# Performance work log

Measured on AMD Instinct MI355X. Metric: run time of the kernel, lower is better.

The kernel has to match this reference:

```python
import jax, jax.numpy as jnp
import numpy as np

B, L, D = 32, 128, 512

def setup_inputs() -> dict:
    key = jax.random.key(0)
    ks = jax.random.split(key, 10)
    s = 1.0 / np.sqrt(D)
    return {
        "current_sotw": jax.random.normal(ks[0], (B, L, D), jnp.float32),
        "new_obs": jax.random.normal(ks[1], (B, L, D), jnp.float32),
        "Wq": jax.random.uniform(ks[2], (D, D), jnp.float32, -s, s),   # linear_query weight
        "bq": jax.random.uniform(ks[3], (D,), jnp.float32, -s, s),     # linear_query bias
        "Wc": jax.random.uniform(ks[4], (D, D), jnp.float32, -s, s),   # linear_context (no bias)
        "v": jax.random.uniform(ks[5], (D,), jnp.float32, -s, s),      # v projection to scalar score
        "Wout": jax.random.uniform(ks[6], (2 * D, D), jnp.float32, -s, s),  # linear_out weight
        "bout": jax.random.uniform(ks[7], (D,), jnp.float32, -s, s),        # linear_out bias (mlp type)
        "mix": jax.random.uniform(ks[8], (1,), jnp.float32),           # mixing_proportion ~ U[0,1)
    }

def _global_attn_mlp(source, memory, Wq, bq, Wc, v, Wout, bout):
    # OpenNMT GlobalAttention, attn_type='mlp', attn_func='softmax'
    wq = jnp.einsum('btd,de->bte', source, Wq) + bq          # [B,T,D]
    uh = jnp.einsum('bsd,de->bse', memory, Wc)               # [B,S,D]
    # scores: v . tanh(wq + uh) over broadcast [B,T,S,D]
    scores = jnp.einsum('btsd,d->bts', jnp.tanh(wq[:, :, None, :] + uh[:, None, :, :]), v)
    align = jax.nn.softmax(scores, axis=-1)                  # [B,T,S]
    c = jnp.einsum('bts,bsd->btd', align, memory)            # context [B,T,D]
    attn_h = jnp.einsum('btd,de->bte', jnp.concatenate([c, source], axis=-1), Wout) + bout
    return attn_h  # [B,T,D] (the torch code transposes to [T,B,D] then back)

def reference(current_sotw, new_obs, Wq, bq, Wc, v, Wout, bout, mix):
    a1 = _global_attn_mlp(new_obs, current_sotw, Wq, bq, Wc, v, Wout, bout)
    a2 = _global_attn_mlp(current_sotw, new_obs, Wq, bq, Wc, v, Wout, bout)
    m = mix[0]
    return (1.0 - m) * a1 + m * a2
```

## Files before the change

### kernel.cpp

```cpp
#include <hip/hip_runtime.h>

#define DD 512
#define SS 128
#define TT4 4
#define SCH16 16
#define RW 520
#define C2F 2.8853900817779268f
#define L2EF 1.4426950408889634f

typedef __bf16 bf16x8 __attribute__((ext_vector_type(8)));
typedef float f32x4 __attribute__((ext_vector_type(4)));
typedef unsigned int uint32x4 __attribute__((ext_vector_type(4)));

__device__ __forceinline__ unsigned short f2bf(float f) {
    unsigned int u = __builtin_bit_cast(unsigned int, f);
    u += 0x7fffu + ((u >> 16) & 1u);
    return (unsigned short)(u >> 16);
}
__device__ __forceinline__ float bflo(unsigned int u) { return __builtin_bit_cast(float, u << 16); }
__device__ __forceinline__ float bfhi(unsigned int u) { return __builtin_bit_cast(float, u & 0xffff0000u); }

__global__ __launch_bounds__(256)
void cvt_dual(const float* __restrict__ a, const float* __restrict__ b,
              unsigned short* __restrict__ oa, unsigned short* __restrict__ ob, int n8)
{
    int i = blockIdx.x * 256 + threadIdx.x;
    const float* in; unsigned short* out; int k;
    if (i < n8) { in = a; out = oa; k = i; }
    else        { in = b; out = ob; k = i - n8; }
    const float4 x = ((const float4*)in)[2 * k];
    const float4 y = ((const float4*)in)[2 * k + 1];
    uint32x4 o;
    o[0] = (unsigned)f2bf(x.x) | ((unsigned)f2bf(x.y) << 16);
    o[1] = (unsigned)f2bf(x.z) | ((unsigned)f2bf(x.w) << 16);
    o[2] = (unsigned)f2bf(y.x) | ((unsigned)f2bf(y.y) << 16);
    o[3] = (unsigned)f2bf(y.z) | ((unsigned)f2bf(y.w) << 16);
    ((uint32x4*)out)[k] = o;
}

__global__ __launch_bounds__(256)
void transpose_all(const float* __restrict__ Wq, const float* __restrict__ Wc,
                   const float* __restrict__ Wout,
                   unsigned short* __restrict__ Wqct, unsigned short* __restrict__ Woutt)
{
    __shared__ float t[64][65];
    const int z = blockIdx.z;
    const float* in; unsigned short* out; int R, r0;
    if (z == 0)      { in = Wq;   out = Wqct;             R = 512;  r0 = blockIdx.y * 64; }
    else if (z == 1) { in = Wc;   out = Wqct + 512 * 512; R = 512;  r0 = blockIdx.y * 64; }
    else             { in = Wout; out = Woutt;            R = 1024; r0 = (z - 2) * 512 + blockIdx.y * 64; }
    const int c0 = blockIdx.x * 64;
    const int tid = threadIdx.x;
    const int lc = tid & 63, lr = tid >> 6;
    #pragma unroll
    for (int i = 0; i < 16; ++i) {
        int r = lr + i * 4;
        t[r][lc] = in[(size_t)(r0 + r) * 512 + c0 + lc];
    }
    __syncthreads();
    #pragma unroll
    for (int i = 0; i < 16; ++i) {
        int rr = lr + i * 4;
        out[(size_t)(c0 + rr) * R + r0 + lc] = f2bf(t[lc][rr]);
    }
}

__global__ __launch_bounds__(256)
void gemm_proj(const unsigned short* __restrict__ A0, const unsigned short* __restrict__ A1,
               const unsigned short* __restrict__ Bt, const float* __restrict__ bq,
               unsigned short* __restrict__ w0, unsigned short* __restrict__ u0,
               unsigned short* __restrict__ w1, unsigned short* __restrict__ u1)
{
    constexpr int K = 512, LDA = 72;
    __shared__ __align__(16) unsigned short As[128][LDA];
    __shared__ __align__(16) unsigned short Bs[128][LDA];

    const unsigned short* A = blockIdx.z ? A1 : A0;
    unsigned short* outW    = blockIdx.z ? w1 : w0;
    unsigned short* outU    = blockIdx.z ? u1 : u0;

    const int tid = threadIdx.x;
    const int n0 = blockIdx.x * 128, m0 = blockIdx.y * 128;
    const int lane = tid & 63, wid = tid >> 6;
    const int wr = wid >> 1, wc = wid & 1;
    const int lr = lane & 15, kb = lane >> 4;

    f32x4 acc[4][4] = {};
    uint32x4 ra[4], rb[4];

    auto LOADK = [&](int k0) {
        #pragma unroll
        for (int j = 0; j < 4; ++j) {
            int id = tid + 256 * j; int r = id >> 3, s = id & 7;
            ra[j] = *(const uint32x4*)&A[(size_t)(m0 + r) * K + k0 + s * 8];
            rb[j] = *(const uint32x4*)&Bt[(size_t)(n0 + r) * K + k0 + s * 8];
        }
    };

    LOADK(0);
    #pragma unroll 1
    for (int step = 0; step < K / 64; ++step) {
        __syncthreads();
        #pragma unroll
        for (int j = 0; j < 4; ++j) {
            int id = tid + 256 * j; int r = id >> 3, s = id & 7;
            *(uint32x4*)&As[r][s * 8] = ra[j];
            *(uint32x4*)&Bs[r][s * 8] = rb[j];
        }
        __syncthreads();
        if (step + 1 < K / 64) LOADK((step + 1) * 64);
        #pragma unroll
        for (int kk = 0; kk < 64; kk += 32) {
            bf16x8 bfr[4];
            #pragma unroll
            for (int nf = 0; nf < 4; ++nf)
                bfr[nf] = __builtin_bit_cast(bf16x8, *(const uint32x4*)&Bs[wc * 64 + nf * 16 + lr][kk + kb * 8]);
            #pragma unroll
            for (int mf = 0; mf < 4; ++mf) {
                bf16x8 a0 = __builtin_bit_cast(bf16x8, *(const uint32x4*)&As[wr * 64 + mf * 16 + lr][kk + kb * 8]);
                #pragma unroll
                for (int nf = 0; nf < 4; ++nf)
                    acc[mf][nf] = __builtin_amdgcn_mfma_f32_16x16x32_bf16(a0, bfr[nf], acc[mf][nf], 0, 0, 0);
            }
        }
    }

    #pragma unroll
    for (int nf = 0; nf < 4; ++nf) {
        const int col = n0 + wc * 64 + nf * 16 + lr;
        const float bv = (col < 512) ? bq[col] : 0.0f;
        #pragma unroll
        for (int mf = 0; mf < 4; ++mf) {
            const int row = m0 + wr * 64 + mf * 16 + kb * 4;
            #pragma unroll
            for (int r = 0; r < 4; ++r) {
                const float valf = acc[mf][nf][r];
                if (col < 512) outW[(size_t)(row + r) * 512 + col] = f2bf((valf + bv) * C2F);
                else           outU[(size_t)(row + r) * 512 + (col - 512)] = f2bf(valf * C2F);
            }
        }
    }
}

__global__ __launch_bounds__(256)
void gemm_final(const unsigned short* __restrict__ c1, const unsigned short* __restrict__ c2,
                const float* __restrict__ no, const float* __restrict__ cs,
                const float* __restrict__ mix, const unsigned short* __restrict__ Bt,
                const float* __restrict__ bout, float* __restrict__ out)
{
    constexpr int K = 1024, LDA = 72;
    __shared__ __align__(16) unsigned short As[128][LDA];
    __shared__ __align__(16) unsigned short Bs[64][LDA];

    const int tid = threadIdx.x;
    const int n0 = blockIdx.x * 64, m0 = blockIdx.y * 128;
    const int lane = tid & 63, wid = tid >> 6;
    const int wr = wid >> 1, wc = wid & 1;
    const int lr = lane & 15, kb = lane >> 4;
    const float mxv = mix[0], omv = 1.0f - mxv;

    f32x4 acc[4][2] = {};
    uint32x4 ra[4], rb[2];

    auto LOADK = [&](int k0) {
        #pragma unroll
        for (int j = 0; j < 4; ++j) {
            int id = tid + 256 * j; int r = id >> 3, s = id & 7;
            const size_t row = m0 + r;
            const int k = k0 + s * 8;
            uint32x4 o;
            if (k < 512) {
                const uint32x4 x1 = *(const uint32x4*)&c1[row * 512 + k];
                const uint32x4 x2 = *(const uint32x4*)&c2[row * 512 + k];
                #pragma unroll
                for (int q = 0; q < 4; ++q) {
                    float lo = omv * bflo(x1[q]) + mxv * bflo(x2[q]);
                    float hi = omv * bfhi(x1[q]) + mxv * bfhi(x2[q]);
                    o[q] = (unsigned)f2bf(lo) | ((unsigned)f2bf(hi) << 16);
                }
            } else {
                const float* n1 = &no[row * 512 + k - 512];
                const float* s1 = &cs[row * 512 + k - 512];
                const float4 a1 = *(const float4*)n1, a2 = *(const float4*)(n1 + 4);
                const float4 b1 = *(const float4*)s1, b2 = *(const float4*)(s1 + 4);
                o[0] = (unsigned)f2bf(omv * a1.x + mxv * b1.x) | ((unsigned)f2bf(omv * a1.y + mxv * b1.y) << 16);
                o[1] = (unsigned)f2bf(omv * a1.z + mxv * b1.z) | ((unsigned)f2bf(omv * a1.w + mxv * b1.w) << 16);
                o[2] = (unsigned)f2bf(omv * a2.x + mxv * b2.x) | ((unsigned)f2bf(omv * a2.y + mxv * b2.y) << 16);
                o[3] = (unsigned)f2bf(omv * a2.z + mxv * b2.z) | ((unsigned)f2bf(omv * a2.w + mxv * b2.w) << 16);
            }
            ra[j] = o;
        }
        #pragma unroll
        for (int j = 0; j < 2; ++j) {
            int id = tid + 256 * j; int r = id >> 3, s = id & 7;
            rb[j] = *(const uint32x4*)&Bt[(size_t)(n0 + r) * K + k0 + s * 8];
        }
    };

    LOADK(0);
    #pragma unroll 1
    for (int step = 0; step < K / 64; ++step) {
        __syncthreads();
        #pragma unroll
        for (int j = 0; j < 4; ++j) {
            int id = tid + 256 * j; int r = id >> 3, s = id & 7;
            *(uint32x4*)&As[r][s * 8] = ra[j];
        }
        #pragma unroll
        for (int j = 0; j < 2; ++j) {
            int id = tid + 256 * j; int r = id >> 3, s = id & 7;
            *(uint32x4*)&Bs[r][s * 8] = rb[j];
        }
        __syncthreads();
        if (step + 1 < K / 64) LOADK((step + 1) * 64);
        #pragma unroll
        for (int kk = 0; kk < 64; kk += 32) {
            bf16x8 b0 = __builtin_bit_cast(bf16x8, *(const uint32x4*)&Bs[wc * 32 + lr][kk + kb * 8]);
            bf16x8 b1 = __builtin_bit_cast(bf16x8, *(const uint32x4*)&Bs[wc * 32 + 16 + lr][kk + kb * 8]);
            #pragma unroll
            for (int mf = 0; mf < 4; ++mf) {
                bf16x8 a0 = __builtin_bit_cast(bf16x8, *(const uint32x4*)&As[wr * 64 + mf * 16 + lr][kk + kb * 8]);
                acc[mf][0] = __builtin_amdgcn_mfma_f32_16x16x32_bf16(a0, b0, acc[mf][0], 0, 0, 0);
                acc[mf][1] = __builtin_amdgcn_mfma_f32_16x16x32_bf16(a0, b1, acc[mf][1], 0, 0, 0);
            }
        }
    }

    #pragma unroll
    for (int nf = 0; nf < 2; ++nf) {
        const int col = n0 + wc * 32 + nf * 16 + lr;
        const float bv = bout[col];
        #pragma unroll
        for (int mf = 0; mf < 4; ++mf) {
            const int row = m0 + wr * 64 + mf * 16 + kb * 4;
            #pragma unroll
            for (int r = 0; r < 4; ++r)
                out[(size_t)(row + r) * 512 + col] = acc[mf][nf][r] + bv;
        }
    }
}

__global__ __launch_bounds__(512, 8)
void attn_fused(const unsigned short* __restrict__ wq,
                const unsigned short* __restrict__ uh,
                const float* __restrict__ v,
                const unsigned short* __restrict__ mem,
                unsigned short* __restrict__ c_out)
{
    __shared__ __align__(16) unsigned short s_ew[TT4 * RW];
    __shared__ __align__(16) unsigned short s_eu[SCH16 * RW];
    __shared__ __align__(16) unsigned short s_v2[DD];
    __shared__ __align__(16) float s_sc[TT4 * SS];

    const int b = blockIdx.y, t0 = blockIdx.x * TT4;
    const int tid = threadIdx.x;

    if (tid < 256) {
        const int row = tid >> 6, G = tid & 63;
        const uint32x4 w4 = *(const uint32x4*)&wq[((size_t)b * SS + t0 + row) * DD + G * 8];
        uint32x4 o;
        #pragma unroll
        for (int q = 0; q < 4; ++q) {
            const float e0 = __builtin_amdgcn_exp2f(bflo(w4[q]));
            const float e1 = __builtin_amdgcn_exp2f(bfhi(w4[q]));
            o[q] = (unsigned)f2bf(e0) | ((unsigned)f2bf(e1) << 16);
        }
        *(uint32x4*)&s_ew[row * RW + G * 8] = o;
    } else if (tid < 320) {
        const int H = tid - 256;
        const float4 p = *(const float4*)&v[H * 8];
        const float4 q = *(const float4*)&v[H * 8 + 4];
        uint32x4 o;
        o[0] = (unsigned)f2bf(p.x * 2.f) | ((unsigned)f2bf(p.y * 2.f) << 16);
        o[1] = (unsigned)f2bf(p.z * 2.f) | ((unsigned)f2bf(p.w * 2.f) << 16);
        o[2] = (unsigned)f2bf(q.x * 2.f) | ((unsigned)f2bf(q.y * 2.f) << 16);
        o[3] = (unsigned)f2bf(q.z * 2.f) | ((unsigned)f2bf(q.w * 2.f) << 16);
        *(uint32x4*)&s_v2[H * 8] = o;
    }

    const int oct = tid & 7;
    const int sr  = (tid >> 3) & 15;
    const int t   = tid >> 7;

    for (int sc0 = 0; sc0 < SS; sc0 += SCH16) {
        __syncthreads();
        {
            int i = tid;
            #pragma unroll
            for (int rep = 0; rep < 2; ++rep, i += 512) {
                const int row = i >> 6, G = i & 63;
                const uint32x4 u4 = *(const uint32x4*)&uh[((size_t)b * SS + sc0 + row) * DD + G * 8];
                uint32x4 o;
                #pragma unroll
                for (int q = 0; q < 4; ++q) {
                    const unsigned e0 = __builtin_bit_cast(unsigned, __builtin_amdgcn_exp2f(bflo(u4[q])));
                    const unsigned e1 = __builtin_bit_cast(unsigned, __builtin_amdgcn_exp2f(bfhi(u4[q])));
                    o[q] = (e0 >> 16) | (e1 & 0xffff0000u);
                }
                *(uint32x4*)&s_eu[row * RW + G * 8] = o;
            }
        }
        __syncthreads();

        const unsigned short* wrow = &s_ew[t * RW];
        const unsigned short* urow = &s_eu[sr * RW];

        float a0 = 0.f, a1 = 0.f, a2 = 0.f, a3 = 0.f;
        #pragma unroll
        for (int j = 0; j < 8; ++j) {
            const int ch = (8 * j + oct) * 8;
            const uint32x4 w4 = *(const uint32x4*)&wrow[ch];
            const uint32x4 u4 = *(const uint32x4*)&urow[ch];
            const uint32x4 v4 = *(const uint32x4*)&s_v2[ch];
            a0 = fmaf(bflo(v4[0]), __builtin_amdgcn_rcpf(fmaf(bflo(w4[0]), bflo(u4[0]), 1.f)), a0);
            a1 = fmaf(bfhi(v4[0]), __builtin_amdgcn_rcpf(fmaf(bfhi(w4[0]), bfhi(u4[0]), 1.f)), a1);
            a2 = fmaf(bflo(v4[1]), __builtin_amdgcn_rcpf(fmaf(bflo(w4[1]), bflo(u4[1]), 1.f)), a2);
            a3 = fmaf(bfhi(v4[1]), __builtin_amdgcn_rcpf(fmaf(bfhi(w4[1]), bfhi(u4[1]), 1.f)), a3);
            a0 = fmaf(bflo(v4[2]), __builtin_amdgcn_rcpf(fmaf(bflo(w4[2]), bflo(u4[2]), 1.f)), a0);
            a1 = fmaf(bfhi(v4[2]), __builtin_amdgcn_rcpf(fmaf(bfhi(w4[2]), bfhi(u4[2]), 1.f)), a1);
            a2 = fmaf(bflo(v4[3]), __builtin_amdgcn_rcpf(fmaf(bflo(w4[3]), bflo(u4[3]), 1.f)), a2);
            a3 = fmaf(bfhi(v4[3]), __builtin_amdgcn_rcpf(fmaf(bfhi(w4[3]), bfhi(u4[3]), 1.f)), a3);
        }
        float p = (a0 + a1) + (a2 + a3);
        p += __shfl_xor(p, 1);
        p += __shfl_xor(p, 2);
        p += __shfl_xor(p, 4);
        if (oct == 0) s_sc[t * SS + sc0 + sr] = -p;
    }
    __syncthreads();

    if (tid < 128) {
        const int tr = tid >> 5, l32 = tid & 31;
        float x0 = s_sc[tr * SS + l32];
        float x1 = s_sc[tr * SS + l32 + 32];
        float x2 = s_sc[tr * SS + l32 + 64];
        float x3 = s_sc[tr * SS + l32 + 96];
        float mx = fmaxf(fmaxf(x0, x1), fmaxf(x2, x3));
        #pragma unroll
        for (int off = 16; off > 0; off >>= 1) mx = fmaxf(mx, __shfl_xor(mx, off));
        const float e0 = __builtin_amdgcn_exp2f((x0 - mx) * L2EF);
        const float e1 = __builtin_amdgcn_exp2f((x1 - mx) * L2EF);
        const float e2 = __builtin_amdgcn_exp2f((x2 - mx) * L2EF);
        const float e3 = __builtin_amdgcn_exp2f((x3 - mx) * L2EF);
        float sum = (e0 + e1) + (e2 + e3);
        #pragma unroll
        for (int off = 16; off > 0; off >>= 1) sum += __shfl_xor(sum, off);
        const float rs = __builtin_amdgcn_rcpf(sum);
        s_sc[tr * SS + l32]      = e0 * rs;
        s_sc[tr * SS + l32 + 32] = e1 * rs;
        s_sc[tr * SS + l32 + 64] = e2 * rs;
        s_sc[tr * SS + l32 + 96] = e3 * rs;
    }
    __syncthreads();

    {
        const int w = tid >> 6, lane = tid & 63;
        const int tb = w & 3, half = w >> 2;
        const int d = half * 256 + lane * 4;
        const unsigned short* mb = mem + (size_t)b * SS * DD + d;
        f32x4 ac = {0.f, 0.f, 0.f, 0.f};
        #pragma unroll 1
        for (int s = 0; s < SS; s += 4) {
            const float4 e4 = *(const float4*)&s_sc[tb * SS + s];
            #pragma unroll
            for (int q = 0; q < 4; ++q) {
                const float e = (q == 0) ? e4.x : (q == 1) ? e4.y : (q == 2) ? e4.z : e4.w;
                const uint2 mv = *(const uint2*)&mb[(size_t)(s + q) * DD];
                ac[0] = fmaf(e, bflo(mv.x), ac[0]);
                ac[1] = fmaf(e, bfhi(mv.x), ac[1]);
                ac[2] = fmaf(e, bflo(mv.y), ac[2]);
                ac[3] = fmaf(e, bfhi(mv.y), ac[3]);
            }
        }
        uint2 st;
        st.x = (unsigned)f2bf(ac[0]) | ((unsigned)f2bf(ac[1]) << 16);
        st.y = (unsigned)f2bf(ac[2]) | ((unsigned)f2bf(ac[3]) << 16);
        *(uint2*)&c_out[((size_t)b * SS + t0 + tb) * DD + d] = st;
    }
}

extern "C" void kernel_launch(void* const* d_in, const int* in_sizes, int n_in,
                              void* d_out, int out_size, void* d_ws, size_t ws_size,
                              hipStream_t stream) {
    const float* cs   = (const float*)d_in[0];
    const float* no   = (const float*)d_in[1];
    const float* Wq   = (const float*)d_in[2];
    const float* bq   = (const float*)d_in[3];
    const float* Wc   = (const float*)d_in[4];
    const float* v    = (const float*)d_in[5];
    const float* Wout = (const float*)d_in[6];
    const float* bout = (const float*)d_in[7];
    const float* mix  = (const float*)d_in[8];
    float* out = (float*)d_out;

    typedef unsigned short us;
    char* ws = (char*)d_ws;
    us* cs_bf = (us*)(ws);
    us* no_bf = (us*)(ws + (4u  << 20));
    us* Wqct  = (us*)(ws + (8u  << 20));
    us* Woutt = (us*)(ws + (9u  << 20));
    us* wq1   = (us*)(ws + (10u << 20));
    us* uh2   = (us*)(ws + (14u << 20));
    us* wq2   = (us*)(ws + (18u << 20));
    us* uh1   = (us*)(ws + (22u << 20));
    us* c1    = (us*)(ws + (26u << 20));
    us* c2    = (us*)(ws + (10u << 20));

    const dim3 b256(256);
    const int n8 = 4096 * DD / 8;

    cvt_dual<<<dim3(2 * n8 / 256), b256, 0, stream>>>(cs, no, cs_bf, no_bf, n8);
    transpose_all<<<dim3(8, 8, 4), b256, 0, stream>>>(Wq, Wc, Wout, Wqct, Woutt);

    gemm_proj<<<dim3(8, 32, 2), b256, 0, stream>>>(no_bf, cs_bf, Wqct, bq,
                                                   wq1, uh2, wq2, uh1);

    attn_fused<<<dim3(32, 32), dim3(512), 0, stream>>>(wq1, uh1, v, cs_bf, c1);
    attn_fused<<<dim3(32, 32), dim3(512), 0, stream>>>(wq2, uh2, v, no_bf, c2);

    gemm_final<<<dim3(8, 32), b256, 0, stream>>>(c1, c2, no, cs, mix, Woutt, bout, out);
}
```

Measured before the change: 302.9 us.

## Merge attention launches, store exp tables in fp32, pair reciprocals per element pair

The two attention launches become one grid with a z dimension that selects the direction. c2 gets its own workspace slot because it can no longer alias wq1 while both directions run together. The exp(wq) and exp(uh) tables and v now live in shared memory as fp32 instead of bf16, and the uh chunk shrinks from 16 to 8 rows. The inner loop combines two terms v_a/p_a + v_b/p_b into a single reciprocal of p_a*p_b, which halves the rcp instructions at the cost of extra multiplies. The risks are more shared memory traffic per element and overflow in the product p_a*p_b for large exponent values.

Result: faster. 285.5 us (-5.7%).

```diff
diff --git a/kernel.cpp b/kernel.cpp
--- a/kernel.cpp
+++ b/kernel.cpp
@@ -3,8 +3,8 @@
 #define DD 512
 #define SS 128
 #define TT4 4
-#define SCH16 16
-#define RW 520
+#define SCH8 8
+#define RWF 516
 #define C2F 2.8853900817779268f
 #define L2EF 1.4426950408889634f
 
@@ -241,16 +241,22 @@
 }
 
 __global__ __launch_bounds__(512, 8)
-void attn_fused(const unsigned short* __restrict__ wq,
-                const unsigned short* __restrict__ uh,
-                const float* __restrict__ v,
-                const unsigned short* __restrict__ mem,
-                unsigned short* __restrict__ c_out)
+void attn_fused(const unsigned short* __restrict__ wqA, const unsigned short* __restrict__ uhA,
+                const unsigned short* __restrict__ memA, unsigned short* __restrict__ coutA,
+                const unsigned short* __restrict__ wqB, const unsigned short* __restrict__ uhB,
+                const unsigned short* __restrict__ memB, unsigned short* __restrict__ coutB,
+                const float* __restrict__ v)
 {
-    __shared__ __align__(16) unsigned short s_ew[TT4 * RW];
-    __shared__ __align__(16) unsigned short s_eu[SCH16 * RW];
-    __shared__ __align__(16) unsigned short s_v2[DD];
+    __shared__ __align__(16) float s_ew[TT4 * RWF];
+    __shared__ __align__(16) float s_eu[SCH8 * RWF];
+    __shared__ __align__(16) float s_v2[DD];
     __shared__ __align__(16) float s_sc[TT4 * SS];
+
+    const int z = blockIdx.z;
+    const unsigned short* wq  = z ? wqB  : wqA;
+    const unsigned short* uh  = z ? uhB  : uhA;
+    const unsigned short* mem = z ? memB : memA;
+    unsigned short* c_out     = z ? coutB : coutA;
 
     const int b = blockIdx.y, t0 = blockIdx.x * TT4;
     const int tid = threadIdx.x;
@@ -258,74 +264,70 @@
     if (tid < 256) {
         const int row = tid >> 6, G = tid & 63;
         const uint32x4 w4 = *(const uint32x4*)&wq[((size_t)b * SS + t0 + row) * DD + G * 8];
-        uint32x4 o;
-        #pragma unroll
-        for (int q = 0; q < 4; ++q) {
-            const float e0 = __builtin_amdgcn_exp2f(bflo(w4[q]));
-            const float e1 = __builtin_amdgcn_exp2f(bfhi(w4[q]));
-            o[q] = (unsigned)f2bf(e0) | ((unsigned)f2bf(e1) << 16);
-        }
-        *(uint32x4*)&s_ew[row * RW + G * 8] = o;
+        f32x4 o0, o1;
+        o0[0] = __builtin_amdgcn_exp2f(bflo(w4[0])); o0[1] = __builtin_amdgcn_exp2f(bfhi(w4[0]));
+        o0[2] = __builtin_amdgcn_exp2f(bflo(w4[1])); o0[3] = __builtin_amdgcn_exp2f(bfhi(w4[1]));
+        o1[0] = __builtin_amdgcn_exp2f(bflo(w4[2])); o1[1] = __builtin_amdgcn_exp2f(bfhi(w4[2]));
+        o1[2] = __builtin_amdgcn_exp2f(bflo(w4[3])); o1[3] = __builtin_amdgcn_exp2f(bfhi(w4[3]));
+        *(f32x4*)&s_ew[row * RWF + G * 8]     = o0;
+        *(f32x4*)&s_ew[row * RWF + G * 8 + 4] = o1;
     } else if (tid < 320) {
         const int H = tid - 256;
-        const float4 p = *(const float4*)&v[H * 8];
-        const float4 q = *(const float4*)&v[H * 8 + 4];
-        uint32x4 o;
-        o[0] = (unsigned)f2bf(p.x * 2.f) | ((unsigned)f2bf(p.y * 2.f) << 16);
-        o[1] = (unsigned)f2bf(p.z * 2.f) | ((unsigned)f2bf(p.w * 2.f) << 16);
-        o[2] = (unsigned)f2bf(q.x * 2.f) | ((unsigned)f2bf(q.y * 2.f) << 16);
-        o[3] = (unsigned)f2bf(q.z * 2.f) | ((unsigned)f2bf(q.w * 2.f) << 16);
-        *(uint32x4*)&s_v2[H * 8] = o;
-    }
-
-    const int oct = tid & 7;
-    const int sr  = (tid >> 3) & 15;
-    const int t   = tid >> 7;
-
-    for (int sc0 = 0; sc0 < SS; sc0 += SCH16) {
+        float4 p = *(const float4*)&v[H * 8];
+        float4 q = *(const float4*)&v[H * 8 + 4];
+        p.x *= 2.f; p.y *= 2.f; p.z *= 2.f; p.w *= 2.f;
+        q.x *= 2.f; q.y *= 2.f; q.z *= 2.f; q.w *= 2.f;
+        *(float4*)&s_v2[H * 8]     = p;
+        *(float4*)&s_v2[H * 8 + 4] = q;
+    }
+
+    const int oct4 = tid & 15;
+    const int sr   = (tid >> 4) & 7;
+    const int t    = tid >> 7;
+
+    for (int sc0 = 0; sc0 < SS; sc0 += SCH8) {
         __syncthreads();
         {
-            int i = tid;
-            #pragma unroll
-            for (int rep = 0; rep < 2; ++rep, i += 512) {
-                const int row = i >> 6, G = i & 63;
-                const uint32x4 u4 = *(const uint32x4*)&uh[((size_t)b * SS + sc0 + row) * DD + G * 8];
-                uint32x4 o;
-                #pragma unroll
-                for (int q = 0; q < 4; ++q) {
-                    const unsigned e0 = __builtin_bit_cast(unsigned, __builtin_amdgcn_exp2f(bflo(u4[q])));
-                    const unsigned e1 = __builtin_bit_cast(unsigned, __builtin_amdgcn_exp2f(bfhi(u4[q])));
-                    o[q] = (e0 >> 16) | (e1 & 0xffff0000u);
-                }
-                *(uint32x4*)&s_eu[row * RW + G * 8] = o;
-            }
-        }
-        __syncthreads();
-
-        const unsigned short* wrow = &s_ew[t * RW];
-        const unsigned short* urow = &s_eu[sr * RW];
-
-        float a0 = 0.f, a1 = 0.f, a2 = 0.f, a3 = 0.f;
+            #pragma unroll
+            for (int rep = 0; rep < 2; ++rep) {
+                const int idx = tid + rep * 512;
+                const int row = idx >> 7, c = idx & 127;
+                const uint2 u2 = *(const uint2*)&uh[((size_t)b * SS + sc0 + row) * DD + c * 4];
+                f32x4 o;
+                o[0] = __builtin_amdgcn_exp2f(bflo(u2.x));
+                o[1] = __builtin_amdgcn_exp2f(bfhi(u2.x));
+                o[2] = __builtin_amdgcn_exp2f(bflo(u2.y));
+                o[3] = __builtin_amdgcn_exp2f(bfhi(u2.y));
+                *(f32x4*)&s_eu[row * RWF + c * 4] = o;
+            }
+        }
+        __syncthreads();
+
+        const float* wrow = &s_ew[t * RWF];
+        const float* urow = &s_eu[sr * RWF];
+
+        float a0 = 0.f, a1 = 0.f;
         #pragma unroll
         for (int j = 0; j < 8; ++j) {
-            const int ch = (8 * j + oct) * 8;
-            const uint32x4 w4 = *(const uint32x4*)&wrow[ch];
-            const uint32x4 u4 = *(const uint32x4*)&urow[ch];
-            const uint32x4 v4 = *(const uint32x4*)&s_v2[ch];
-            a0 = fmaf(bflo(v4[0]), __builtin_amdgcn_rcpf(fmaf(bflo(w4[0]), bflo(u4[0]), 1.f)), a0);
-            a1 = fmaf(bfhi(v4[0]), __builtin_amdgcn_rcpf(fmaf(bfhi(w4[0]), bfhi(u4[0]), 1.f)), a1);
-            a2 = fmaf(bflo(v4[1]), __builtin_amdgcn_rcpf(fmaf(bflo(w4[1]), bflo(u4[1]), 1.f)), a2);
-            a3 = fmaf(bfhi(v4[1]), __builtin_amdgcn_rcpf(fmaf(bfhi(w4[1]), bfhi(u4[1]), 1.f)), a3);
-            a0 = fmaf(bflo(v4[2]), __builtin_amdgcn_rcpf(fmaf(bflo(w4[2]), bflo(u4[2]), 1.f)), a0);
-            a1 = fmaf(bfhi(v4[2]), __builtin_amdgcn_rcpf(fmaf(bfhi(w4[2]), bfhi(u4[2]), 1.f)), a1);
-            a2 = fmaf(bflo(v4[3]), __builtin_amdgcn_rcpf(fmaf(bflo(w4[3]), bflo(u4[3]), 1.f)), a2);
-            a3 = fmaf(bfhi(v4[3]), __builtin_amdgcn_rcpf(fmaf(bfhi(w4[3]), bfhi(u4[3]), 1.f)), a3);
-        }
-        float p = (a0 + a1) + (a2 + a3);
+            const int cf = (16 * j + oct4) * 4;
+            const f32x4 w4 = *(const f32x4*)&wrow[cf];
+            const f32x4 u4 = *(const f32x4*)&urow[cf];
+            const f32x4 v4 = *(const f32x4*)&s_v2[cf];
+            const float p0 = fmaf(w4[0], u4[0], 1.f);
+            const float p1 = fmaf(w4[1], u4[1], 1.f);
+            float n0 = v4[0] * p1; n0 = fmaf(v4[1], p0, n0);
+            a0 = fmaf(n0, __builtin_amdgcn_rcpf(p0 * p1), a0);
+            const float p2 = fmaf(w4[2], u4[2], 1.f);
+            const float p3 = fmaf(w4[3], u4[3], 1.f);
+            float n1 = v4[2] * p3; n1 = fmaf(v4[3], p2, n1);
+            a1 = fmaf(n1, __builtin_amdgcn_rcpf(p2 * p3), a1);
+        }
+        float p = a0 + a1;
         p += __shfl_xor(p, 1);
         p += __shfl_xor(p, 2);
         p += __shfl_xor(p, 4);
-        if (oct == 0) s_sc[t * SS + sc0 + sr] = -p;
+        p += __shfl_xor(p, 8);
+        if (oct4 == 0) s_sc[t * SS + sc0 + sr] = -p;
     }
     __syncthreads();
 
@@ -404,7 +406,7 @@
     us* wq2   = (us*)(ws + (18u << 20));
     us* uh1   = (us*)(ws + (22u << 20));
     us* c1    = (us*)(ws + (26u << 20));
-    us* c2    = (us*)(ws + (10u << 20));
+    us* c2    = (us*)(ws + (30u << 20));
 
     const dim3 b256(256);
     const int n8 = 4096 * DD / 8;
@@ -415,8 +417,8 @@
     gemm_proj<<<dim3(8, 32, 2), b256, 0, stream>>>(no_bf, cs_bf, Wqct, bq,
                                                    wq1, uh2, wq2, uh1);
 
-    attn_fused<<<dim3(32, 32), dim3(512), 0, stream>>>(wq1, uh1, v, cs_bf, c1);
-    attn_fused<<<dim3(32, 32), dim3(512), 0, stream>>>(wq2, uh2, v, no_bf, c2);
+    attn_fused<<<dim3(32, 32, 2), dim3(512), 0, stream>>>(wq1, uh1, cs_bf, c1,
+                                                          wq2, uh2, no_bf, c2, v);
 
     gemm_final<<<dim3(8, 32), b256, 0, stream>>>(c1, c2, no, cs, mix, Woutt, bout, out);
 }
```
